# Kernel tuning notes

Hardware: AMD Instinct MI355X
Metric: run time of the kernel (lower is better)

The kernel has to match this reference:

```python
import jax, jax.numpy as jnp
import numpy as np

B, C, N = 8, 128, 256          # batch, descriptor dim, num points
DIMS = [2 * C, 512, 256, 64, 1]  # [input_dim] + cfg.layers + [1]
EPS = 1e-5


def setup_inputs() -> dict:
    key = jax.random.key(0)
    ks = jax.random.split(key, 32)
    inp = {"x": jax.random.normal(ks[0], (B, C, N), dtype=jnp.float32)}
    ki = 1
    for li in range(4):
        cin, cout = DIMS[li], DIMS[li + 1]
        inp[f"W{li+1}"] = jax.random.normal(ks[ki], (cout, cin), dtype=jnp.float32) / np.sqrt(cin); ki += 1
        inp[f"b{li+1}"] = jnp.zeros((cout,), dtype=jnp.float32)
        if li < 3:  # BatchNorm only on hidden layers
            inp[f"g{li+1}"] = jnp.ones((cout,), dtype=jnp.float32)
            inp[f"be{li+1}"] = jnp.zeros((cout,), dtype=jnp.float32)
            inp[f"m{li+1}"] = 0.1 * jax.random.normal(ks[ki], (cout,), dtype=jnp.float32); ki += 1
            inp[f"v{li+1}"] = 0.5 + jax.random.uniform(ks[ki], (cout,), dtype=jnp.float32); ki += 1
    return inp


def _bn(h, g, be, m, v):
    # inference-mode BatchNorm1d over channel axis of (b, c, p)
    scale = (g * jax.lax.rsqrt(v + EPS))[None, :, None]
    return (h - m[None, :, None]) * scale + be[None, :, None]


def _conv1x1(h, W, b):
    # Conv1d kernel_size=1 == channel matmul: (o,c),(b,c,p)->(b,o,p)
    return jnp.einsum('oc,bcp->bop', W, h) + b[None, :, None]


def reference(x, W1, b1, g1, be1, m1, v1, W2, b2, g2, be2, m2, v2,
              W3, b3, g3, be3, m3, v3, W4, b4):
    b, c, n = x.shape
    # pairwise concat: inputs[:, :, i*n+j] = cat(x[:,:,i], x[:,:,j])
    xi = jnp.broadcast_to(x[:, :, :, None], (b, c, n, n))  # varies with i
    xj = jnp.broadcast_to(x[:, :, None, :], (b, c, n, n))  # varies with j
    pair = jnp.concatenate([xi, xj], axis=1).reshape(b, 2 * c, n * n)
    h = jax.nn.relu(_bn(_conv1x1(pair, W1, b1), g1, be1, m1, v1))
    h = jax.nn.relu(_bn(_conv1x1(h, W2, b2), g2, be2, m2, v2))
    h = jax.nn.relu(_bn(_conv1x1(h, W3, b3), g3, be3, m3, v3))
    h = _conv1x1(h, W4, b4)
    return jax.nn.sigmoid(h)  # (b, 1, n*n) == edges_pred
```

## Files before the change

### kernel.cpp

```cpp
#include <hip/hip_runtime.h>
#include <hip/hip_bf16.h>
#include <hip/hip_fp16.h>

typedef _Float16 f16x8 __attribute__((ext_vector_type(8)));
typedef _Float16 f16x4 __attribute__((ext_vector_type(4)));
typedef float    f32x4 __attribute__((ext_vector_type(4)));

#define EPSV 1e-5f

__global__ void prep_convert(const float* __restrict__ W2, const float* __restrict__ W3,
                             const float* __restrict__ b2, const float* __restrict__ g2,
                             const float* __restrict__ be2, const float* __restrict__ m2,
                             const float* __restrict__ v2,
                             const float* __restrict__ b3, const float* __restrict__ g3,
                             const float* __restrict__ be3, const float* __restrict__ m3,
                             const float* __restrict__ v3,
                             _Float16* __restrict__ W2T, _Float16* __restrict__ W3h,
                             float* __restrict__ sc2, float* __restrict__ sh2,
                             float* __restrict__ sc3, float* __restrict__ sh3) {
  int tid = blockIdx.x * 256 + threadIdx.x;
  if (blockIdx.x == 0) {
    int t = threadIdx.x;
    if (t < 256) { float s = g2[t] * rsqrtf(v2[t] + EPSV); sc2[t] = s; sh2[t] = be2[t] + (b2[t] - m2[t]) * s; }
    if (t < 64)  { float s = g3[t] * rsqrtf(v3[t] + EPSV); sc3[t] = s; sh3[t] = be3[t] + (b3[t] - m3[t]) * s; }
  }
  {
    int lane = tid & 63, cg = (tid >> 6) & 15, ks = tid >> 10;
    int ch = cg * 16 + (lane & 15);
    int k  = ks * 32 + (lane >> 4) * 8;
    const float* src = W2 + (size_t)ch * 512 + k;
    f16x8 v;
    #pragma unroll
    for (int e = 0; e < 8; ++e) v[e] = (_Float16)src[e];
    *(f16x8*)(W2T + (size_t)tid * 8) = v;
  }
  W3h[tid] = (_Float16)W3[tid];
}

__global__ void prep_ab(const float* __restrict__ x, const float* __restrict__ W1,
                        const float* __restrict__ b1, const float* __restrict__ g1,
                        const float* __restrict__ be1, const float* __restrict__ m1,
                        const float* __restrict__ v1,
                        _Float16* __restrict__ Ap, _Float16* __restrict__ Bp) {
  int b  = blockIdx.x >> 7;
  int og = blockIdx.x & 127;
  int i  = threadIdx.x;
  float accA[4] = {0.f, 0.f, 0.f, 0.f};
  float accB[4] = {0.f, 0.f, 0.f, 0.f};
  const float* xb  = x  + (size_t)b * 128 * 256 + i;
  const float* w1r = W1 + (size_t)og * 4 * 256;
  #pragma unroll 8
  for (int c = 0; c < 128; ++c) {
    float xa = xb[c * 256];
    #pragma unroll
    for (int oo = 0; oo < 4; ++oo) {
      accA[oo] = fmaf(w1r[oo * 256 + c],       xa, accA[oo]);
      accB[oo] = fmaf(w1r[oo * 256 + 128 + c], xa, accB[oo]);
    }
  }
  f16x4 oa, ob;
  {
    int o0 = og * 4;
    #pragma unroll
    for (int oo = 0; oo < 4; ++oo) {
      float s = g1[o0 + oo] * rsqrtf(v1[o0 + oo] + EPSV);
      float h = be1[o0 + oo] + (b1[o0 + oo] - m1[o0 + oo]) * s;
      oa[oo] = (_Float16)(accA[oo] * s + h);
      ob[oo] = (_Float16)(accB[oo] * s);
    }
  }
  size_t base = ((size_t)(b * 256 + i) << 9) + og * 4;
  *(f16x4*)(Ap + base) = oa;
  *(f16x4*)(Bp + base) = ob;
}

struct alignas(16) Smem {
  union {
    struct { _Float16 sA[16][552]; _Float16 sB[8][552]; } s2;
    struct { _Float16 h2[64][264]; float part[4][64]; } e;
  } u;
};

__global__ __launch_bounds__(256, 2) void edge_main(
    const _Float16* __restrict__ Ap, const _Float16* __restrict__ Bp,
    const _Float16* __restrict__ W2T, const _Float16* __restrict__ W3h,
    const float* __restrict__ sc2, const float* __restrict__ sh2,
    const float* __restrict__ sc3, const float* __restrict__ sh3,
    const float* __restrict__ W4, const float* __restrict__ b4,
    float* __restrict__ out) {
  __shared__ Smem sm;
  const int blk = blockIdx.x;
  const int b  = blk >> 9;
  const int it = (blk >> 5) & 15;
  const int jt = blk & 31;
  const int i0 = it * 16, j0 = jt * 8;

  const int t    = threadIdx.x;
  const int w    = t >> 6;
  const int lane = t & 63;
  const int llo  = lane & 15;
  const int lhi  = lane >> 4;
  const int gj   = llo & 7;
  const int giOff= llo >> 3;
  const int chH  = w & 1;
  const int ptH  = w >> 1;
  const int aBase= ptH * 8;

  {
    int ra = t >> 4, ca = (t & 15) * 32;
    const _Float16* src = Ap + ((size_t)(b * 256 + i0 + ra) << 9) + ca;
    #pragma unroll
    for (int s = 0; s < 4; ++s)
      *(f16x8*)&sm.u.s2.sA[ra][ca + s * 8] = *(const f16x8*)(src + s * 8);
    int rb = t >> 5, cb = (t & 31) * 16;
    const _Float16* srcb = Bp + ((size_t)(b * 256 + j0 + rb) << 9) + cb;
    #pragma unroll
    for (int s = 0; s < 2; ++s)
      *(f16x8*)&sm.u.s2.sB[rb][cb + s * 8] = *(const f16x8*)(srcb + s * 8);
  }

  const f32x4 vzero = {0.f, 0.f, 0.f, 0.f};
  f32x4 acc[8][4];
  #pragma unroll
  for (int mt = 0; mt < 8; ++mt)
    #pragma unroll
    for (int nt = 0; nt < 4; ++nt) acc[mt][nt] = vzero;

  const f16x8 z8 = {};
  const _Float16* w2base = W2T + chH * 4096 + lane * 8;

#define LOAD_AF(dst, kk)                                                     \
  {                                                                          \
    const _Float16* _p = w2base + (kk) * 8192;                               \
    _Pragma("unroll")                                                        \
    for (int mt = 0; mt < 8; ++mt)                                           \
      dst[mt] = *(const f16x8*)(_p + mt * 512);                              \
  }

#define KSTEP(afv, kk)                                                       \
  {                                                                          \
    const int k0 = (kk) * 32 + lhi * 8;                                      \
    f16x8 bv = *(const f16x8*)&sm.u.s2.sB[gj][k0];                           \
    f16x8 bfr[4];                                                            \
    _Pragma("unroll")                                                        \
    for (int nt = 0; nt < 4; ++nt) {                                         \
      f16x8 av = *(const f16x8*)&sm.u.s2.sA[aBase + nt * 2 + giOff][k0];     \
      f16x8 sv = av + bv;                                                    \
      bfr[nt] = __builtin_elementwise_max(sv, z8);                           \
    }                                                                        \
    _Pragma("unroll")                                                        \
    for (int mt = 0; mt < 8; ++mt)                                           \
      _Pragma("unroll")                                                      \
      for (int nt = 0; nt < 4; ++nt)                                         \
        acc[mt][nt] = __builtin_amdgcn_mfma_f32_16x16x32_f16(                \
            afv[mt], bfr[nt], acc[mt][nt], 0, 0, 0);                         \
  }

  f16x8 afA[8], afB[8];
  LOAD_AF(afA, 0);

  __syncthreads();

  for (int ks = 0; ks < 16; ks += 2) {
    LOAD_AF(afB, ks + 1);
    KSTEP(afA, ks);
    if (ks + 2 < 16) LOAD_AF(afA, ks + 2);
    KSTEP(afB, ks + 1);
  }
#undef LOAD_AF
#undef KSTEP

  __syncthreads();

  #pragma unroll
  for (int pass = 0; pass < 2; ++pass) {
    if (ptH == pass) {
      #pragma unroll
      for (int mt = 0; mt < 8; ++mt) {
        int ch = chH * 128 + mt * 16 + lhi * 4;
        float4 s = *(const float4*)(sc2 + ch);
        float4 h = *(const float4*)(sh2 + ch);
        #pragma unroll
        for (int nt = 0; nt < 4; ++nt) {
          int pt = nt * 16 + llo;
          f32x4 a = acc[mt][nt];
          f16x4 hb;
          hb[0] = (_Float16)fmaxf(fmaf(a[0], s.x, h.x), 0.f);
          hb[1] = (_Float16)fmaxf(fmaf(a[1], s.y, h.y), 0.f);
          hb[2] = (_Float16)fmaxf(fmaf(a[2], s.z, h.z), 0.f);
          hb[3] = (_Float16)fmaxf(fmaf(a[3], s.w, h.w), 0.f);
          *(f16x4*)&sm.u.e.h2[pt][ch] = hb;
        }
      }
    }
    __syncthreads();

    {
      f32x4 acc3[4];
      #pragma unroll
      for (int nt = 0; nt < 4; ++nt) acc3[nt] = vzero;
      const _Float16* w3p = W3h + (size_t)(w * 16 + llo) * 256 + lhi * 8;
      #pragma unroll
      for (int k8 = 0; k8 < 8; ++k8) {
        f16x8 a3 = *(const f16x8*)(w3p + k8 * 32);
        #pragma unroll
        for (int nt = 0; nt < 4; ++nt) {
          f16x8 b3 = *(const f16x8*)&sm.u.e.h2[nt * 16 + llo][k8 * 32 + lhi * 8];
          acc3[nt] = __builtin_amdgcn_mfma_f32_16x16x32_f16(a3, b3, acc3[nt], 0, 0, 0);
        }
      }
      int ch3 = w * 16 + lhi * 4;
      float4 s  = *(const float4*)(sc3 + ch3);
      float4 h  = *(const float4*)(sh3 + ch3);
      float4 wv = *(const float4*)(W4 + ch3);
      #pragma unroll
      for (int nt = 0; nt < 4; ++nt) {
        float p = fmaxf(fmaf(acc3[nt][0], s.x, h.x), 0.f) * wv.x
                + fmaxf(fmaf(acc3[nt][1], s.y, h.y), 0.f) * wv.y
                + fmaxf(fmaf(acc3[nt][2], s.z, h.z), 0.f) * wv.z
                + fmaxf(fmaf(acc3[nt][3], s.w, h.w), 0.f) * wv.w;
        p += __shfl_xor(p, 16);
        p += __shfl_xor(p, 32);
        if (lane < 16) sm.u.e.part[w][nt * 16 + llo] = p;
      }
    }
    __syncthreads();

    if (t < 64) {
      float tot = sm.u.e.part[0][t] + sm.u.e.part[1][t] + sm.u.e.part[2][t]
                + sm.u.e.part[3][t] + b4[0];
      float sg = 1.f / (1.f + __expf(-tot));
      int il = pass * 8 + (t >> 3), jl = t & 7;
      out[(size_t)b * 65536 + (size_t)(i0 + il) * 256 + (j0 + jl)] = sg;
    }
    __syncthreads();
  }
}

extern "C" void kernel_launch(void* const* d_in, const int* in_sizes, int n_in,
                              void* d_out, int out_size, void* d_ws, size_t ws_size,
                              hipStream_t stream) {
  const float* x   = (const float*)d_in[0];
  const float* W1  = (const float*)d_in[1];
  const float* b1  = (const float*)d_in[2];
  const float* g1  = (const float*)d_in[3];
  const float* be1 = (const float*)d_in[4];
  const float* m1  = (const float*)d_in[5];
  const float* v1  = (const float*)d_in[6];
  const float* W2  = (const float*)d_in[7];
  const float* b2  = (const float*)d_in[8];
  const float* g2  = (const float*)d_in[9];
  const float* be2 = (const float*)d_in[10];
  const float* m2  = (const float*)d_in[11];
  const float* v2  = (const float*)d_in[12];
  const float* W3  = (const float*)d_in[13];
  const float* b3  = (const float*)d_in[14];
  const float* g3  = (const float*)d_in[15];
  const float* be3 = (const float*)d_in[16];
  const float* m3  = (const float*)d_in[17];
  const float* v3  = (const float*)d_in[18];
  const float* W4  = (const float*)d_in[19];
  const float* b4  = (const float*)d_in[20];

  _Float16* Ap = (_Float16*)d_ws;
  _Float16* Bp = Ap + 1048576;
  float* sc2 = (float*)(Bp + 1048576);
  float* sh2 = sc2 + 256;
  float* sc3 = sh2 + 256;
  float* sh3 = sc3 + 64;
  _Float16* W2T = (_Float16*)(sh3 + 64);
  _Float16* W3h = W2T + 131072;

  prep_convert<<<64, 256, 0, stream>>>(W2, W3, b2, g2, be2, m2, v2,
                                       b3, g3, be3, m3, v3,
                                       W2T, W3h, sc2, sh2, sc3, sh3);
  prep_ab<<<1024, 256, 0, stream>>>(x, W1, b1, g1, be1, m1, v1, Ap, Bp);
  edge_main<<<4096, 256, 0, stream>>>(Ap, Bp, W2T, W3h, sc2, sh2, sc3, sh3, W4, b4, (float*)d_out);
}
```

Measured before the change: 168.9 us.

## Process all 128 points in one epilogue pass and relayout W2T per channel half

Replaces the two-pass layer-3 epilogue, where each half of the points was staged separately, with a single pass that stages all 128 points' layer-2 activations in shared memory. Each wave then runs 8 MFMA tiles against one W3 fragment per k-step, and the block issues one reduction and one output store. This removes several block barriers and reloads of W3, sc3, sh3 and W4. The W2T prep layout is changed so each channel half is contiguous per k-step. The larger h2 buffer raises shared-memory use, which may affect occupancy at two blocks per CU.

```diff
diff --git a/kernel.cpp b/kernel.cpp
--- a/kernel.cpp
+++ b/kernel.cpp
@@ -25,8 +25,11 @@
     if (t < 64)  { float s = g3[t] * rsqrtf(v3[t] + EPSV); sc3[t] = s; sh3[t] = be3[t] + (b3[t] - m3[t]) * s; }
   }
   {
-    int lane = tid & 63, cg = (tid >> 6) & 15, ks = tid >> 10;
-    int ch = cg * 16 + (lane & 15);
+    int lane = tid & 63;
+    int mt   = (tid >> 6) & 7;
+    int ks   = (tid >> 9) & 15;
+    int chH  = (tid >> 13) & 1;
+    int ch = (chH * 8 + mt) * 16 + (lane & 15);
     int k  = ks * 32 + (lane >> 4) * 8;
     const float* src = W2 + (size_t)ch * 512 + k;
     f16x8 v;
@@ -77,7 +80,7 @@
 struct alignas(16) Smem {
   union {
     struct { _Float16 sA[16][552]; _Float16 sB[8][552]; } s2;
-    struct { _Float16 h2[64][264]; float part[4][64]; } e;
+    struct { _Float16 h2[128][264]; float part[4][128]; } e;
   } u;
 };
 
@@ -127,11 +130,11 @@
     for (int nt = 0; nt < 4; ++nt) acc[mt][nt] = vzero;
 
   const f16x8 z8 = {};
-  const _Float16* w2base = W2T + chH * 4096 + lane * 8;
+  const _Float16* w2base = W2T + chH * 65536 + lane * 8;
 
 #define LOAD_AF(dst, kk)                                                     \
   {                                                                          \
-    const _Float16* _p = w2base + (kk) * 8192;                               \
+    const _Float16* _p = w2base + (kk) * 4096;                               \
     _Pragma("unroll")                                                        \
     for (int mt = 0; mt < 8; ++mt)                                           \
       dst[mt] = *(const f16x8*)(_p + mt * 512);                              \
@@ -173,67 +176,60 @@
   __syncthreads();
 
   #pragma unroll
-  for (int pass = 0; pass < 2; ++pass) {
-    if (ptH == pass) {
+  for (int mt = 0; mt < 8; ++mt) {
+    int ch = chH * 128 + mt * 16 + lhi * 4;
+    float4 s = *(const float4*)(sc2 + ch);
+    float4 h = *(const float4*)(sh2 + ch);
+    #pragma unroll
+    for (int nt = 0; nt < 4; ++nt) {
+      int pt = ptH * 64 + nt * 16 + llo;
+      f32x4 a = acc[mt][nt];
+      f16x4 hb;
+      hb[0] = (_Float16)fmaxf(fmaf(a[0], s.x, h.x), 0.f);
+      hb[1] = (_Float16)fmaxf(fmaf(a[1], s.y, h.y), 0.f);
+      hb[2] = (_Float16)fmaxf(fmaf(a[2], s.z, h.z), 0.f);
+      hb[3] = (_Float16)fmaxf(fmaf(a[3], s.w, h.w), 0.f);
+      *(f16x4*)&sm.u.e.h2[pt][ch] = hb;
+    }
+  }
+  __syncthreads();
+
+  {
+    f32x4 acc3[8];
+    #pragma unroll
+    for (int nt2 = 0; nt2 < 8; ++nt2) acc3[nt2] = vzero;
+    const _Float16* w3p = W3h + (size_t)(w * 16 + llo) * 256 + lhi * 8;
+    #pragma unroll
+    for (int k8 = 0; k8 < 8; ++k8) {
+      f16x8 a3 = *(const f16x8*)(w3p + k8 * 32);
       #pragma unroll
-      for (int mt = 0; mt < 8; ++mt) {
-        int ch = chH * 128 + mt * 16 + lhi * 4;
-        float4 s = *(const float4*)(sc2 + ch);
-        float4 h = *(const float4*)(sh2 + ch);
-        #pragma unroll
-        for (int nt = 0; nt < 4; ++nt) {
-          int pt = nt * 16 + llo;
-          f32x4 a = acc[mt][nt];
-          f16x4 hb;
-          hb[0] = (_Float16)fmaxf(fmaf(a[0], s.x, h.x), 0.f);
-          hb[1] = (_Float16)fmaxf(fmaf(a[1], s.y, h.y), 0.f);
-          hb[2] = (_Float16)fmaxf(fmaf(a[2], s.z, h.z), 0.f);
-          hb[3] = (_Float16)fmaxf(fmaf(a[3], s.w, h.w), 0.f);
-          *(f16x4*)&sm.u.e.h2[pt][ch] = hb;
-        }
+      for (int nt2 = 0; nt2 < 8; ++nt2) {
+        f16x8 b3 = *(const f16x8*)&sm.u.e.h2[nt2 * 16 + llo][k8 * 32 + lhi * 8];
+        acc3[nt2] = __builtin_amdgcn_mfma_f32_16x16x32_f16(a3, b3, acc3[nt2], 0, 0, 0);
       }
     }
-    __syncthreads();
-
-    {
-      f32x4 acc3[4];
-      #pragma unroll
-      for (int nt = 0; nt < 4; ++nt) acc3[nt] = vzero;
-      const _Float16* w3p = W3h + (size_t)(w * 16 + llo) * 256 + lhi * 8;
-      #pragma unroll
-      for (int k8 = 0; k8 < 8; ++k8) {
-        f16x8 a3 = *(const f16x8*)(w3p + k8 * 32);
-        #pragma unroll
-        for (int nt = 0; nt < 4; ++nt) {
-          f16x8 b3 = *(const f16x8*)&sm.u.e.h2[nt * 16 + llo][k8 * 32 + lhi * 8];
-          acc3[nt] = __builtin_amdgcn_mfma_f32_16x16x32_f16(a3, b3, acc3[nt], 0, 0, 0);
-        }
-      }
-      int ch3 = w * 16 + lhi * 4;
-      float4 s  = *(const float4*)(sc3 + ch3);
-      float4 h  = *(const float4*)(sh3 + ch3);
-      float4 wv = *(const float4*)(W4 + ch3);
-      #pragma unroll
-      for (int nt = 0; nt < 4; ++nt) {
-        float p = fmaxf(fmaf(acc3[nt][0], s.x, h.x), 0.f) * wv.x
-                + fmaxf(fmaf(acc3[nt][1], s.y, h.y), 0.f) * wv.y
-                + fmaxf(fmaf(acc3[nt][2], s.z, h.z), 0.f) * wv.z
-                + fmaxf(fmaf(acc3[nt][3], s.w, h.w), 0.f) * wv.w;
-        p += __shfl_xor(p, 16);
-        p += __shfl_xor(p, 32);
-        if (lane < 16) sm.u.e.part[w][nt * 16 + llo] = p;
-      }
-    }
-    __syncthreads();
-
-    if (t < 64) {
-      float tot = sm.u.e.part[0][t] + sm.u.e.part[1][t] + sm.u.e.part[2][t]
-                + sm.u.e.part[3][t] + b4[0];
-      float sg = 1.f / (1.f + __expf(-tot));
-      int il = pass * 8 + (t >> 3), jl = t & 7;
-      out[(size_t)b * 65536 + (size_t)(i0 + il) * 256 + (j0 + jl)] = sg;
-    }
-    __syncthreads();
+    int ch3 = w * 16 + lhi * 4;
+    float4 s  = *(const float4*)(sc3 + ch3);
+    float4 h  = *(const float4*)(sh3 + ch3);
+    float4 wv = *(const float4*)(W4 + ch3);
+    #pragma unroll
+    for (int nt2 = 0; nt2 < 8; ++nt2) {
+      float p = fmaxf(fmaf(acc3[nt2][0], s.x, h.x), 0.f) * wv.x
+              + fmaxf(fmaf(acc3[nt2][1], s.y, h.y), 0.f) * wv.y
+              + fmaxf(fmaf(acc3[nt2][2], s.z, h.z), 0.f) * wv.z
+              + fmaxf(fmaf(acc3[nt2][3], s.w, h.w), 0.f) * wv.w;
+      p += __shfl_xor(p, 16);
+      p += __shfl_xor(p, 32);
+      if (lane < 16) sm.u.e.part[w][nt2 * 16 + llo] = p;
+    }
+  }
+  __syncthreads();
+
+  if (t < 128) {
+    float tot = sm.u.e.part[0][t] + sm.u.e.part[1][t] + sm.u.e.part[2][t]
+              + sm.u.e.part[3][t] + b4[0];
+    float sg = 1.f / (1.f + __expf(-tot));
+    out[(size_t)b * 65536 + (size_t)(i0 + (t >> 3)) * 256 + (j0 + (t & 7))] = sg;
   }
 }
 
```

Result: faster. 160.5 us (-5.0%).
